# Kernel tuning notes

Hardware: AMD Instinct MI355X
Metric: run time of the kernel (lower is better)

Reference implementation:

```python
import jax, jax.numpy as jnp
import numpy as np

LN_EPS = 1e-5

def _ln(x, g, b):
    mu = x.mean(-1, keepdims=True)
    var = ((x - mu) ** 2).mean(-1, keepdims=True)
    return (x - mu) / jnp.sqrt(var + LN_EPS) * g + b

def setup_inputs() -> dict:
    B, T, S, H, A = 512, 512, 64, 128, 8
    key = jax.random.key(0)
    ks = jax.random.split(key, 8)
    def rn(k, shape, s=0.1):
        return jax.random.normal(k, shape, jnp.float32) * s
    return {
        'x_seq': jax.random.normal(ks[0], (B, T, S), jnp.float32),
        'hx': jnp.zeros((1, B, H), jnp.float32),
        'done_seq': jax.random.randint(ks[1], (B, T), 0, 2, jnp.int32),
        'W_feat': rn(ks[2], (H, S)), 'b_feat': jnp.zeros((H,), jnp.float32),
        'g_f': jnp.ones((H,), jnp.float32), 'beta_f': jnp.zeros((H,), jnp.float32),
        'W_ih': rn(ks[3], (3 * H, H)), 'W_hh': rn(ks[4], (3 * H, H)),
        'b_ih': jnp.zeros((3 * H,), jnp.float32), 'b_hh': jnp.zeros((3 * H,), jnp.float32),
        'g_r': jnp.ones((H,), jnp.float32), 'beta_r': jnp.zeros((H,), jnp.float32),
        'W_pol': rn(ks[5], (A, H)), 'b_pol': jnp.zeros((A,), jnp.float32),
        'W_val': rn(ks[6], (1, H)), 'b_val': jnp.zeros((1,), jnp.float32),
    }

def reference(x_seq, hx, done_seq, W_feat, b_feat, g_f, beta_f,
              W_ih, W_hh, b_ih, b_hh, g_r, beta_r,
              W_pol, b_pol, W_val, b_val):
    # feature: Linear -> LayerNorm -> ReLU (no time dependence, vectorized over T)
    z = jax.nn.relu(_ln(jnp.einsum('bts,hs->bth', x_seq, W_feat) + b_feat, g_f, beta_f))
    # precompute input-side GRU gates for all timesteps: (B, T, 3H)
    gx = jnp.einsum('bth,gh->btg', z, W_ih) + b_ih
    done = done_seq.astype(x_seq.dtype)

    def step(h, inp):
        gx_t, d_t = inp  # (B,3H), (B,)
        gh = h @ W_hh.T + b_hh
        xr, xz, xn = jnp.split(gx_t, 3, axis=-1)
        hr, hz, hn = jnp.split(gh, 3, axis=-1)
        r = jax.nn.sigmoid(xr + hr)
        u = jax.nn.sigmoid(xz + hz)
        n = jnp.tanh(xn + r * hn)
        h_new = (1.0 - u) * n + u * h  # PyTorch GRU cell update
        y = _ln(h_new, g_r, beta_r)    # ln_rnn applied to output only
        logits = y @ W_pol.T + b_pol
        value = y @ W_val.T + b_val
        h_next = h_new * (1.0 - d_t)[:, None]  # done-mask reset of carried state
        return h_next, (logits, value)

    h_fin, (logits, values) = jax.lax.scan(
        step, hx[0], (gx.transpose(1, 0, 2), done.T))
    # scan outputs are (T,B,...); return batch-first like the torch module
    return logits.transpose(1, 0, 2), values.transpose(1, 0, 2), h_fin[None]
```

## Files before the change

kernel.cpp:

```cpp
#include <hip/hip_runtime.h>


typedef _Float16 h2t __attribute__((ext_vector_type(2)));
typedef _Float16 f16x4 __attribute__((ext_vector_type(4)));
typedef _Float16 f16x8 __attribute__((ext_vector_type(8)));
typedef float f32x4 __attribute__((ext_vector_type(4)));

#define BAR() __asm__ volatile("s_waitcnt lgkmcnt(0)\n\ts_barrier" ::: "memory")

#define BB 512
#define TT 512
#define SS 64
#define HH 128
#define AA 8
#define CK 16
#define NCK (TT / CK)
#define VALO (BB * TT * AA)
#define HFIN (VALO + BB * TT)

__global__ void __launch_bounds__(256, 2) p1_kernel(
    const float* __restrict__ x,   const float* __restrict__ Wf,
    const float* __restrict__ bfe, const float* __restrict__ gf,
    const float* __restrict__ btf, const float* __restrict__ Wih,
    const float* __restrict__ bih, unsigned short* __restrict__ gxws)
{
    const int tid = threadIdx.x;
    const int wv  = tid >> 6;
    const int l   = tid & 63;
    const int lo  = l & 15;
    const int hi  = l >> 4;
    const size_t m0 = (size_t)blockIdx.x * 64;

    __shared__ __align__(16) _Float16 xh[64][72];
    __shared__ __align__(16) float    fb[64][132];
    __shared__ __align__(16) _Float16 zh[64][136];

    {
        const int r  = tid >> 2;
        const int c0 = (tid & 3) << 4;
        const float4* px = (const float4*)(x + (m0 + (size_t)r) * SS + c0);
        float4 a = px[0], b = px[1], c = px[2], d = px[3];
        f16x8 h0, h1;
        h0[0]=(_Float16)a.x; h0[1]=(_Float16)a.y; h0[2]=(_Float16)a.z; h0[3]=(_Float16)a.w;
        h0[4]=(_Float16)b.x; h0[5]=(_Float16)b.y; h0[6]=(_Float16)b.z; h0[7]=(_Float16)b.w;
        h1[0]=(_Float16)c.x; h1[1]=(_Float16)c.y; h1[2]=(_Float16)c.z; h1[3]=(_Float16)c.w;
        h1[4]=(_Float16)d.x; h1[5]=(_Float16)d.y; h1[6]=(_Float16)d.z; h1[7]=(_Float16)d.w;
        *(f16x8*)&xh[r][c0]     = h0;
        *(f16x8*)&xh[r][c0 + 8] = h1;
    }
    __syncthreads();

    {
        const int n0 = wv << 5;
        f32x4 acc[4][2];
        #pragma unroll
        for (int mt = 0; mt < 4; ++mt)
            #pragma unroll
            for (int nt = 0; nt < 2; ++nt) {
                acc[mt][nt][0]=0.f; acc[mt][nt][1]=0.f;
                acc[mt][nt][2]=0.f; acc[mt][nt][3]=0.f;
            }
        #pragma unroll
        for (int kk = 0; kk < 2; ++kk) {
            f16x8 bf[2];
            #pragma unroll
            for (int nt = 0; nt < 2; ++nt) {
                const float4* wp = (const float4*)(Wf + (size_t)(n0 + nt*16 + lo) * SS + kk*32 + hi*8);
                float4 w0 = wp[0], w1 = wp[1];
                f16x8 t;
                t[0]=(_Float16)w0.x; t[1]=(_Float16)w0.y; t[2]=(_Float16)w0.z; t[3]=(_Float16)w0.w;
                t[4]=(_Float16)w1.x; t[5]=(_Float16)w1.y; t[6]=(_Float16)w1.z; t[7]=(_Float16)w1.w;
                bf[nt] = t;
            }
            #pragma unroll
            for (int mt = 0; mt < 4; ++mt) {
                f16x8 af = *(const f16x8*)&xh[mt*16 + lo][kk*32 + hi*8];
                acc[mt][0] = __builtin_amdgcn_mfma_f32_16x16x32_f16(af, bf[0], acc[mt][0], 0, 0, 0);
                acc[mt][1] = __builtin_amdgcn_mfma_f32_16x16x32_f16(af, bf[1], acc[mt][1], 0, 0, 0);
            }
        }
        const float b0 = bfe[n0 + lo];
        const float b1 = bfe[n0 + 16 + lo];
        #pragma unroll
        for (int mt = 0; mt < 4; ++mt)
            #pragma unroll
            for (int j = 0; j < 4; ++j) {
                fb[mt*16 + hi*4 + j][n0 + lo]      = acc[mt][0][j] + b0;
                fb[mt*16 + hi*4 + j][n0 + 16 + lo] = acc[mt][1][j] + b1;
            }
    }
    __syncthreads();

    {
        const int r = tid >> 2;
        const int q = tid & 3;
        const float4* pf = (const float4*)&fb[r][q << 5];
        float4 v[8];
        float s = 0.f, ss = 0.f;
        #pragma unroll
        for (int i = 0; i < 8; ++i) {
            float4 t = pf[i]; v[i] = t;
            s  += (t.x + t.y) + (t.z + t.w);
            ss += (t.x*t.x + t.y*t.y) + (t.z*t.z + t.w*t.w);
        }
        s  += __shfl_xor(s, 1);  s  += __shfl_xor(s, 2);
        ss += __shfl_xor(ss, 1); ss += __shfl_xor(ss, 2);
        const float mu   = s * (1.f / 128.f);
        const float rstd = rsqrtf(ss * (1.f / 128.f) - mu * mu + 1e-5f);
        const float4* pg = (const float4*)(gf  + (q << 5));
        const float4* pb = (const float4*)(btf + (q << 5));
        #pragma unroll
        for (int i = 0; i < 8; ++i) {
            float4 g = pg[i], bb = pb[i], t = v[i];
            h2t pA, pB;
            pA.x = (_Float16)fmaxf((t.x - mu) * rstd * g.x + bb.x, 0.f);
            pA.y = (_Float16)fmaxf((t.y - mu) * rstd * g.y + bb.y, 0.f);
            pB.x = (_Float16)fmaxf((t.z - mu) * rstd * g.z + bb.z, 0.f);
            pB.y = (_Float16)fmaxf((t.w - mu) * rstd * g.w + bb.w, 0.f);
            uint2 u;
            u.x = __builtin_bit_cast(unsigned int, pA);
            u.y = __builtin_bit_cast(unsigned int, pB);
            *(uint2*)&zh[r][(q << 5) + i * 4] = u;
        }
    }
    __syncthreads();

    {
        const int n0 = wv * 96;
        f16x8 bz[4][4];
        #pragma unroll
        for (int mt = 0; mt < 4; ++mt)
            #pragma unroll
            for (int ks = 0; ks < 4; ++ks)
                bz[mt][ks] = *(const f16x8*)&zh[mt*16 + lo][ks*32 + hi*8];
        #pragma unroll
        for (int nt = 0; nt < 6; ++nt) {
            const int nb = n0 + nt * 16;
            const float4 b4 = *(const float4*)(bih + nb + (hi << 2));
            const float* wr = Wih + (size_t)(nb + lo) * HH;
            f32x4 acc[4];
            #pragma unroll
            for (int mt = 0; mt < 4; ++mt) {
                acc[mt][0]=0.f; acc[mt][1]=0.f; acc[mt][2]=0.f; acc[mt][3]=0.f;
            }
            #pragma unroll
            for (int ks = 0; ks < 4; ++ks) {
                const float4* wp = (const float4*)(wr + ks*32 + hi*8);
                float4 w0 = wp[0], w1 = wp[1];
                f16x8 af;
                af[0]=(_Float16)w0.x; af[1]=(_Float16)w0.y; af[2]=(_Float16)w0.z; af[3]=(_Float16)w0.w;
                af[4]=(_Float16)w1.x; af[5]=(_Float16)w1.y; af[6]=(_Float16)w1.z; af[7]=(_Float16)w1.w;
                #pragma unroll
                for (int mt = 0; mt < 4; ++mt)
                    acc[mt] = __builtin_amdgcn_mfma_f32_16x16x32_f16(af, bz[mt][ks], acc[mt], 0, 0, 0);
            }
            #pragma unroll
            for (int mt = 0; mt < 4; ++mt) {
                h2t pA, pB;
                pA.x = (_Float16)(acc[mt][0] + b4.x);
                pA.y = (_Float16)(acc[mt][1] + b4.y);
                pB.x = (_Float16)(acc[mt][2] + b4.z);
                pB.y = (_Float16)(acc[mt][3] + b4.w);
                uint2 u;
                u.x = __builtin_bit_cast(unsigned int, pA);
                u.y = __builtin_bit_cast(unsigned int, pB);
                *(uint2*)(gxws + (m0 + (size_t)(mt*16 + lo)) * 384 + nb + (hi << 2)) = u;
            }
        }
    }
}

__global__ void __launch_bounds__(512, 2) p2_kernel(
    const float* __restrict__ hx,  const int* __restrict__ done,
    const float* __restrict__ Whh, const float* __restrict__ bhh,
    unsigned short* __restrict__ gxws, float* __restrict__ out)
{
    const int tid = threadIdx.x;
    const int blk = blockIdx.x;

    __shared__ __align__(16) _Float16 hsh16[2][2][160];
    __shared__ __align__(16) _Float16 gxb[2][2][CK][384];
    __shared__ float dshf[2][TT];

    const int lo = tid & 15;
    const int hi = (tid & 63) >> 4;
    const int wv = tid >> 6;
    const int Y  = lo & 1;
    const int q  = (lo >> 1) & 3;
    const int du = wv * 16 + hi * 4 + q;
    const bool wr = (lo < 8);
    const bool qb0 = ((lo >> 1) & 1) != 0;
    const bool qb1 = ((lo >> 2) & 1) != 0;

    f16x8 aW[3][4];
    f32x4 bias[3];
    float hp;
    {
        #pragma unroll
        for (int g = 0; g < 3; ++g) {
            const float* wrp = Whh + (size_t)(g * 128 + wv * 16 + lo) * HH;
            #pragma unroll
            for (int ks = 0; ks < 4; ++ks) {
                const float4* wp = (const float4*)(wrp + ks * 32 + hi * 8);
                float4 w0 = wp[0], w1 = wp[1];
                f16x8 t;
                t[0]=(_Float16)w0.x; t[1]=(_Float16)w0.y; t[2]=(_Float16)w0.z; t[3]=(_Float16)w0.w;
                t[4]=(_Float16)w1.x; t[5]=(_Float16)w1.y; t[6]=(_Float16)w1.z; t[7]=(_Float16)w1.w;
                aW[g][ks] = t;
            }
            bias[g] = *(const f32x4*)&bhh[g * 128 + wv * 16 + hi * 4];
        }
        hp = hx[(size_t)(2 * blk + Y) * HH + du];
    }

    if (tid < 256) {
        const int Yc = tid >> 7, d = tid & 127;
        hsh16[0][Yc][d] = (_Float16)hx[(size_t)(2 * blk + Yc) * HH + d];
    }
    for (int idx = tid; idx < 2 * TT; idx += 512)
        dshf[idx >> 9][idx & 511] =
            done[(2 * blk + (idx >> 9)) * TT + (idx & 511)] ? 0.f : 1.f;

    const unsigned short* baseA = gxws + (size_t)(2 * blk + 0) * TT * 384;
    const unsigned short* baseB = gxws + (size_t)(2 * blk + 1) * TT * 384;
    ushort4 rA0, rA1, rA2, rB0, rB1, rB2;
    {
        const ushort4* ca = (const ushort4*)baseA;
        const ushort4* cb = (const ushort4*)baseB;
        rA0=ca[tid]; rA1=ca[512+tid]; rA2=ca[1024+tid];
        rB0=cb[tid]; rB1=cb[512+tid]; rB2=cb[1024+tid];
        ushort4* ga = (ushort4*)&gxb[0][0][0][0];
        ushort4* gb = (ushort4*)&gxb[1][0][0][0];
        ga[tid]=rA0; ga[512+tid]=rA1; ga[1024+tid]=rA2;
        gb[tid]=rB0; gb[512+tid]=rB1; gb[1024+tid]=rB2;
    }
    __syncthreads();

    const _Float16* hbE = &hsh16[0][Y][0];
    const _Float16* hbO = &hsh16[1][Y][0];
    _Float16* hwE = &hsh16[1][Y][du];
    _Float16* hwO = &hsh16[0][Y][du];
    float* hraw = (float*)(gxws + (size_t)(2 * blk + Y) * TT * 384) + du;
    const float* mk = &dshf[Y][0];
    const _Float16* gx0 = &gxb[Y][0][0][du];
    const _Float16* gx1 = &gxb[Y][1][0][du];

    #define GSTEP(HB, HW, MASKT) { \
        f16x8 B0 = *(const f16x8*)&(HB)[0   + hi*8]; \
        f16x8 B1 = *(const f16x8*)&(HB)[32  + hi*8]; \
        f16x8 B2 = *(const f16x8*)&(HB)[64  + hi*8]; \
        f16x8 B3 = *(const f16x8*)&(HB)[96  + hi*8]; \
        const float gr0 = (float)gx[0]; \
        const float gz0 = (float)gx[128]; \
        const float gn0 = (float)gx[256]; \
        const float mask = (MASKT); \
        f32x4 a0 = bias[0], a1 = bias[1], a2 = bias[2]; \
        a0 = __builtin_amdgcn_mfma_f32_16x16x32_f16(aW[0][0], B0, a0, 0, 0, 0); \
        a1 = __builtin_amdgcn_mfma_f32_16x16x32_f16(aW[1][0], B0, a1, 0, 0, 0); \
        a2 = __builtin_amdgcn_mfma_f32_16x16x32_f16(aW[2][0], B0, a2, 0, 0, 0); \
        a0 = __builtin_amdgcn_mfma_f32_16x16x32_f16(aW[0][1], B1, a0, 0, 0, 0); \
        a1 = __builtin_amdgcn_mfma_f32_16x16x32_f16(aW[1][1], B1, a1, 0, 0, 0); \
        a2 = __builtin_amdgcn_mfma_f32_16x16x32_f16(aW[2][1], B1, a2, 0, 0, 0); \
        a0 = __builtin_amdgcn_mfma_f32_16x16x32_f16(aW[0][2], B2, a0, 0, 0, 0); \
        a1 = __builtin_amdgcn_mfma_f32_16x16x32_f16(aW[1][2], B2, a1, 0, 0, 0); \
        a2 = __builtin_amdgcn_mfma_f32_16x16x32_f16(aW[2][2], B2, a2, 0, 0, 0); \
        a0 = __builtin_amdgcn_mfma_f32_16x16x32_f16(aW[0][3], B3, a0, 0, 0, 0); \
        a1 = __builtin_amdgcn_mfma_f32_16x16x32_f16(aW[1][3], B3, a1, 0, 0, 0); \
        a2 = __builtin_amdgcn_mfma_f32_16x16x32_f16(aW[2][3], B3, a2, 0, 0, 0); \
        float xr_a = qb1 ? (qb0 ? a0[3] : a0[2]) : (qb0 ? a0[1] : a0[0]); \
        float xz_a = qb1 ? (qb0 ? a1[3] : a1[2]) : (qb0 ? a1[1] : a1[0]); \
        float hn_a = qb1 ? (qb0 ? a2[3] : a2[2]) : (qb0 ? a2[1] : a2[0]); \
        float xr = gr0 + xr_a; \
        float xz = gz0 + xz_a; \
        float r_ = __builtin_amdgcn_rcpf(1.f + __builtin_amdgcn_exp2f(xr * -1.44269504f)); \
        float u_ = __builtin_amdgcn_rcpf(1.f + __builtin_amdgcn_exp2f(xz * -1.44269504f)); \
        float a_ = gn0 + r_ * hn_a; \
        float F  = __builtin_amdgcn_exp2f(a_ * 2.88539008f); \
        float nn = 1.f - 2.f * __builtin_amdgcn_rcpf(F + 1.f); \
        float hnew = nn + u_ * (hp - nn); \
        hp = hnew * mask; \
        if (wr) { \
            *(HW) = (_Float16)hp; \
            *hraw = hnew; \
        } \
        gx += 384; hraw += 192; \
    }

    for (int c = 0; c < NCK; ++c) {
        if (c + 1 < NCK) {
            const ushort4* ca = (const ushort4*)(baseA + (size_t)(c + 1) * CK * 384);
            const ushort4* cb = (const ushort4*)(baseB + (size_t)(c + 1) * CK * 384);
            rA0=ca[tid]; rA1=ca[512+tid]; rA2=ca[1024+tid];
            rB0=cb[tid]; rB1=cb[512+tid]; rB2=cb[1024+tid];
        }
        const _Float16* gx = (c & 1) ? gx1 : gx0;
        const float* mkc = mk + c * CK;
        #pragma unroll
        for (int jp = 0; jp < CK; jp += 2) {
            GSTEP(hbE, hwE, mkc[jp])
            BAR();
            GSTEP(hbO, hwO, mkc[jp + 1])
            if (jp == CK - 2 && c + 1 < NCK) {
                const int nb = (c + 1) & 1;
                ushort4* ga = (ushort4*)&gxb[0][nb][0][0];
                ushort4* gb = (ushort4*)&gxb[1][nb][0][0];
                ga[tid]=rA0; ga[512+tid]=rA1; ga[1024+tid]=rA2;
                gb[tid]=rB0; gb[512+tid]=rB1; gb[1024+tid]=rB2;
            }
            BAR();
        }
    }

    if (wr)
        out[HFIN + (size_t)(2 * blk + Y) * HH + du] = hp;
}

__global__ void __launch_bounds__(256, 2) p3_kernel(
    const unsigned short* __restrict__ gxws,
    const float* __restrict__ gr,  const float* __restrict__ btr,
    const float* __restrict__ Wp,  const float* __restrict__ bp,
    const float* __restrict__ Wv,  const float* __restrict__ bv,
    float* __restrict__ out)
{
    const int tid = threadIdx.x;
    __shared__ __align__(16) float wpl[9][132];
    __shared__ float bpl[9];

    for (int idx = tid; idx < 9 * HH; idx += 256) {
        int row = idx >> 7, col = idx & 127;
        wpl[row][col] = (row < 8) ? Wp[row * HH + col] : Wv[col];
    }
    if (tid < 9) bpl[tid] = (tid < 8) ? bp[tid] : bv[0];

    const size_t m = (size_t)blockIdx.x * 64 + (tid >> 2);
    const int q = tid & 3;
    const float* hr = (const float*)(gxws + m * 384);

    float4 v[8];
    float s = 0.f, ss = 0.f;
    #pragma unroll
    for (int j = 0; j < 8; ++j) {
        float4 t = ((const float4*)hr)[q + 4 * j];
        v[j] = t;
        s  += (t.x + t.y) + (t.z + t.w);
        ss += (t.x*t.x + t.y*t.y) + (t.z*t.z + t.w*t.w);
    }
    s  += __shfl_xor(s, 1);  s  += __shfl_xor(s, 2);
    ss += __shfl_xor(ss, 1); ss += __shfl_xor(ss, 2);
    const float mu   = s * (1.f / 128.f);
    const float rstd = rsqrtf(ss * (1.f / 128.f) - mu * mu + 1e-5f);

    float4 y[8];
    #pragma unroll
    for (int j = 0; j < 8; ++j) {
        float4 g  = ((const float4*)gr)[q + 4 * j];
        float4 bb = ((const float4*)btr)[q + 4 * j];
        float4 t = v[j];
        y[j].x = (t.x - mu) * rstd * g.x + bb.x;
        y[j].y = (t.y - mu) * rstd * g.y + bb.y;
        y[j].z = (t.z - mu) * rstd * g.z + bb.z;
        y[j].w = (t.w - mu) * rstd * g.w + bb.w;
    }
    __syncthreads();

    float acc[9];
    #pragma unroll
    for (int hd = 0; hd < 9; ++hd) {
        float a = 0.f;
        #pragma unroll
        for (int j = 0; j < 8; ++j) {
            float4 w = ((const float4*)wpl[hd])[q + 4 * j];
            a += (y[j].x * w.x + y[j].y * w.y) + (y[j].z * w.z + y[j].w * w.w);
        }
        acc[hd] = a;
    }
    #pragma unroll
    for (int hd = 0; hd < 9; ++hd) {
        acc[hd] += __shfl_xor(acc[hd], 1);
        acc[hd] += __shfl_xor(acc[hd], 2);
    }
    if (q == 0) {
        float4 o0 = make_float4(acc[0] + bpl[0], acc[1] + bpl[1], acc[2] + bpl[2], acc[3] + bpl[3]);
        float4 o1 = make_float4(acc[4] + bpl[4], acc[5] + bpl[5], acc[6] + bpl[6], acc[7] + bpl[7]);
        ((float4*)(out + m * AA))[0] = o0;
        ((float4*)(out + m * AA))[1] = o1;
    } else if (q == 1) {
        out[VALO + m] = acc[8] + bpl[8];
    }
}

extern "C" void kernel_launch(void* const* d_in, const int* in_sizes, int n_in,
                              void* d_out, int out_size, void* d_ws, size_t ws_size,
                              hipStream_t stream) {
    const float* x   = (const float*)d_in[0];
    const float* hx  = (const float*)d_in[1];
    const int*   dn  = (const int*)d_in[2];
    const float* Wf  = (const float*)d_in[3];
    const float* bfe = (const float*)d_in[4];
    const float* gf  = (const float*)d_in[5];
    const float* btf = (const float*)d_in[6];
    const float* Wih = (const float*)d_in[7];
    const float* Whh = (const float*)d_in[8];
    const float* bih = (const float*)d_in[9];
    const float* bhh = (const float*)d_in[10];
    const float* gr  = (const float*)d_in[11];
    const float* btr = (const float*)d_in[12];
    const float* Wp  = (const float*)d_in[13];
    const float* bp  = (const float*)d_in[14];
    const float* Wv  = (const float*)d_in[15];
    const float* bv  = (const float*)d_in[16];
    float* out = (float*)d_out;

    unsigned short* gxws = (unsigned short*)d_ws;
    hipLaunchKernelGGL(p1_kernel, dim3(BB * TT / 64), dim3(256), 0, stream,
                       x, Wf, bfe, gf, btf, Wih, bih, gxws);
    hipLaunchKernelGGL(p2_kernel, dim3(BB / 2), dim3(512), 0, stream,
                       hx, dn, Whh, bhh, gxws, out);
    hipLaunchKernelGGL(p3_kernel, dim3(BB * TT / 64), dim3(256), 0, stream,
                       gxws, gr, btr, Wp, bp, Wv, bv, out);
}
```

Measured before the change: 506.6 us.

## Process one sequence per block in GRU recurrence to double block count

The recurrent kernel now handles a single batch row per block instead of two, so the grid grows to BB blocks and the launch bound asks for four blocks per multiprocessor. The serial, latency-bound time loop can then have more independent chains resident per CU to hide MFMA, LDS and barrier latency. Shared-memory buffers and the global prefetch shrink to one sequence. The cost is that each MFMA now fills one useful column instead of two, the Whh weight load into registers is repeated by twice as many blocks, and the tighter launch bound may force register spills.

```diff
diff --git a/kernel.cpp b/kernel.cpp
--- a/kernel.cpp
+++ b/kernel.cpp
@@ -170,7 +170,7 @@
     }
 }
 
-__global__ void __launch_bounds__(512, 2) p2_kernel(
+__global__ void __launch_bounds__(512, 4) p2_kernel(
     const float* __restrict__ hx,  const int* __restrict__ done,
     const float* __restrict__ Whh, const float* __restrict__ bhh,
     unsigned short* __restrict__ gxws, float* __restrict__ out)
@@ -178,19 +178,18 @@
     const int tid = threadIdx.x;
     const int blk = blockIdx.x;
 
-    __shared__ __align__(16) _Float16 hsh16[2][2][160];
-    __shared__ __align__(16) _Float16 gxb[2][2][CK][384];
-    __shared__ float dshf[2][TT];
+    __shared__ __align__(16) _Float16 hsh16[2][160];
+    __shared__ __align__(16) _Float16 gxb[2][CK][384];
+    __shared__ float dshf[TT];
 
     const int lo = tid & 15;
     const int hi = (tid & 63) >> 4;
     const int wv = tid >> 6;
-    const int Y  = lo & 1;
-    const int q  = (lo >> 1) & 3;
+    const int q  = lo & 3;
     const int du = wv * 16 + hi * 4 + q;
-    const bool wr = (lo < 8);
-    const bool qb0 = ((lo >> 1) & 1) != 0;
-    const bool qb1 = ((lo >> 2) & 1) != 0;
+    const bool wr = (lo < 4);
+    const bool qb0 = (lo & 1) != 0;
+    const bool qb1 = (lo & 2) != 0;
 
     f16x8 aW[3][4];
     f32x4 bias[3];
@@ -210,40 +209,32 @@
             }
             bias[g] = *(const f32x4*)&bhh[g * 128 + wv * 16 + hi * 4];
         }
-        hp = hx[(size_t)(2 * blk + Y) * HH + du];
-    }
-
-    if (tid < 256) {
-        const int Yc = tid >> 7, d = tid & 127;
-        hsh16[0][Yc][d] = (_Float16)hx[(size_t)(2 * blk + Yc) * HH + d];
-    }
-    for (int idx = tid; idx < 2 * TT; idx += 512)
-        dshf[idx >> 9][idx & 511] =
-            done[(2 * blk + (idx >> 9)) * TT + (idx & 511)] ? 0.f : 1.f;
-
-    const unsigned short* baseA = gxws + (size_t)(2 * blk + 0) * TT * 384;
-    const unsigned short* baseB = gxws + (size_t)(2 * blk + 1) * TT * 384;
-    ushort4 rA0, rA1, rA2, rB0, rB1, rB2;
-    {
-        const ushort4* ca = (const ushort4*)baseA;
-        const ushort4* cb = (const ushort4*)baseB;
-        rA0=ca[tid]; rA1=ca[512+tid]; rA2=ca[1024+tid];
-        rB0=cb[tid]; rB1=cb[512+tid]; rB2=cb[1024+tid];
-        ushort4* ga = (ushort4*)&gxb[0][0][0][0];
-        ushort4* gb = (ushort4*)&gxb[1][0][0][0];
-        ga[tid]=rA0; ga[512+tid]=rA1; ga[1024+tid]=rA2;
-        gb[tid]=rB0; gb[512+tid]=rB1; gb[1024+tid]=rB2;
+        hp = hx[(size_t)blk * HH + du];
+    }
+
+    if (tid < HH)
+        hsh16[0][tid] = (_Float16)hx[(size_t)blk * HH + tid];
+    if (tid < TT)
+        dshf[tid] = done[blk * TT + tid] ? 0.f : 1.f;
+
+    const unsigned short* base = gxws + (size_t)blk * TT * 384;
+    ushort4 rA0, rA1, rA2;
+    {
+        const ushort4* ca = (const ushort4*)base;
+        rA0 = ca[tid]; rA1 = ca[512 + tid]; rA2 = ca[1024 + tid];
+        ushort4* ga = (ushort4*)&gxb[0][0][0];
+        ga[tid] = rA0; ga[512 + tid] = rA1; ga[1024 + tid] = rA2;
     }
     __syncthreads();
 
-    const _Float16* hbE = &hsh16[0][Y][0];
-    const _Float16* hbO = &hsh16[1][Y][0];
-    _Float16* hwE = &hsh16[1][Y][du];
-    _Float16* hwO = &hsh16[0][Y][du];
-    float* hraw = (float*)(gxws + (size_t)(2 * blk + Y) * TT * 384) + du;
-    const float* mk = &dshf[Y][0];
-    const _Float16* gx0 = &gxb[Y][0][0][du];
-    const _Float16* gx1 = &gxb[Y][1][0][du];
+    const _Float16* hbE = &hsh16[0][0];
+    const _Float16* hbO = &hsh16[1][0];
+    _Float16* hwE = &hsh16[1][du];
+    _Float16* hwO = &hsh16[0][du];
+    float* hraw = (float*)(gxws + (size_t)blk * TT * 384) + du;
+    const float* mk = &dshf[0];
+    const _Float16* gx0 = &gxb[0][0][du];
+    const _Float16* gx1 = &gxb[1][0][du];
 
     #define GSTEP(HB, HW, MASKT) { \
         f16x8 B0 = *(const f16x8*)&(HB)[0   + hi*8]; \
@@ -288,10 +279,8 @@
 
     for (int c = 0; c < NCK; ++c) {
         if (c + 1 < NCK) {
-            const ushort4* ca = (const ushort4*)(baseA + (size_t)(c + 1) * CK * 384);
-            const ushort4* cb = (const ushort4*)(baseB + (size_t)(c + 1) * CK * 384);
-            rA0=ca[tid]; rA1=ca[512+tid]; rA2=ca[1024+tid];
-            rB0=cb[tid]; rB1=cb[512+tid]; rB2=cb[1024+tid];
+            const ushort4* ca = (const ushort4*)(base + (size_t)(c + 1) * CK * 384);
+            rA0 = ca[tid]; rA1 = ca[512 + tid]; rA2 = ca[1024 + tid];
         }
         const _Float16* gx = (c & 1) ? gx1 : gx0;
         const float* mkc = mk + c * CK;
@@ -301,18 +290,15 @@
             BAR();
             GSTEP(hbO, hwO, mkc[jp + 1])
             if (jp == CK - 2 && c + 1 < NCK) {
-                const int nb = (c + 1) & 1;
-                ushort4* ga = (ushort4*)&gxb[0][nb][0][0];
-                ushort4* gb = (ushort4*)&gxb[1][nb][0][0];
-                ga[tid]=rA0; ga[512+tid]=rA1; ga[1024+tid]=rA2;
-                gb[tid]=rB0; gb[512+tid]=rB1; gb[1024+tid]=rB2;
+                ushort4* ga = (ushort4*)&gxb[(c + 1) & 1][0][0];
+                ga[tid] = rA0; ga[512 + tid] = rA1; ga[1024 + tid] = rA2;
             }
             BAR();
         }
     }
 
     if (wr)
-        out[HFIN + (size_t)(2 * blk + Y) * HH + du] = hp;
+        out[HFIN + (size_t)blk * HH + du] = hp;
 }
 
 __global__ void __launch_bounds__(256, 2) p3_kernel(
@@ -414,7 +400,7 @@
     unsigned short* gxws = (unsigned short*)d_ws;
     hipLaunchKernelGGL(p1_kernel, dim3(BB * TT / 64), dim3(256), 0, stream,
                        x, Wf, bfe, gf, btf, Wih, bih, gxws);
-    hipLaunchKernelGGL(p2_kernel, dim3(BB / 2), dim3(512), 0, stream,
+    hipLaunchKernelGGL(p2_kernel, dim3(BB), dim3(512), 0, stream,
                        hx, dn, Whh, bhh, gxws, out);
     hipLaunchKernelGGL(p3_kernel, dim3(BB * TT / 64), dim3(256), 0, stream,
                        gxws, gr, btr, Wp, bp, Wv, bv, out);
```

After: 605.9 us. 19.6% more time.
